# Performance work log

Measured on AMD Instinct MI355X. Metric: run time of the kernel, lower is better.

The kernel has to match this reference:

```python
import jax, jax.numpy as jnp
import numpy as np

B=2048; MA=6; S=11; SP=10; D=256; H=4; DH=64; L=12; G=2
NREL=500; NTYPE=1000; NODE=100000; VOC=NODE-NTYPE; NEDGE=100; E=50000; NCLS=NREL+NTYPE
BIG=1e6

def _ln(x, g, b, eps):
    m = jnp.mean(x, -1, keepdims=True)
    v = jnp.var(x, -1, keepdims=True)
    return (x - m) / jnp.sqrt(v + eps) * g + b

def _gat(h, bias, pos, Ws, a_src, a_dst):
    # h: [N,T,D]; bias: [N,T,T] additive mask; pos: [N,T,1] presence mask
    for i in range(Ws.shape[0]):
        hW = h @ Ws[i]                                   # [N,T,D]
        s = hW @ a_src[i]                                # [N,T]
        t = hW @ a_dst[i]                                # [N,T]
        e = jax.nn.leaky_relu(s[:, :, None] + t[:, None, :], 0.2) + bias
        attn = jax.nn.softmax(e, -1)
        h = jax.nn.elu(attn @ hW)
    denom = jnp.clip(jnp.sum(pos, 1), 1.0, None)         # [N,1]
    return jnp.sum(h * pos, 1) / denom                   # masked mean pool -> [N,D]

def _forward(input_ids, input_mask, edge_labels, mask_pos, mask_type, ent_types, groud_truth, l2m,
             node_emb, ln1_g, ln1_b, ln2_g, ln2_b, fc2_bias, fc3_bias, edge_k_emb, edge_v_emb,
             gat1_W, gat1_a_src, gat1_a_dst, gat2_W, gat2_a_src, gat2_a_dst,
             enc_wqkv, enc_wo, enc_ln1g, enc_ln1b, enc_w1, enc_b1, enc_w2, enc_b2, enc_ln2g, enc_ln2b):
    emb_out = _ln(node_emb[input_ids], ln1_g, ln1_b, 1e-12)   # dropout = identity (eval)
    # --- level-1 type hypergraph attention ---
    special = jnp.stack([jnp.full((SP,), 0), jnp.full((SP,), 1), jnp.full((SP,), 2)]).astype(ent_types.dtype)
    type_matrix = jnp.concatenate([special, ent_types[:, 1:]], 0)
    input_type_ids = input_ids[:, 0::2] - NREL                # [B,MA]
    itt = type_matrix[input_type_ids.reshape(-1)]             # [B*MA,SP]
    sgn = jnp.sign(itt).astype(jnp.float32)
    pos = sgn[:, :, None]
    bias = BIG * (pos @ jnp.swapaxes(pos, 1, 2) - 1.0)        # [N,SP,SP]
    input_type = node_emb[itt]                                # [N,SP,D]
    g1 = _gat(input_type, bias, pos, gat1_W, gat1_a_src, gat1_a_dst).reshape(B, MA, D)
    gathered = g1[:, l2m, :].reshape(B * MA, MA - 1, D)       # cross-arity gather
    tmp = jnp.abs(jnp.sum(gathered, 2))                       # [N,MA-1]
    h2 = jnp.concatenate([input_type, gathered], 1)           # [N,SP+MA-1,D]
    sgn2 = jnp.concatenate([sgn, jnp.sign(tmp)], 1)
    pos2 = sgn2[:, :, None]
    bias2 = BIG * (pos2 @ jnp.swapaxes(pos2, 1, 2) - 1.0)
    g2 = _gat(h2, bias2, pos2, gat2_W, gat2_a_src, gat2_a_dst).reshape(B, MA, D)
    emb_out = emb_out.at[:, 0::2, :].set(g2)                  # scatter types into entity slots
    mask_matrix = jnp.where(mask_type == 1, 2, 1)
    emb_out = emb_out.at[jnp.arange(B), mask_pos, :].set(node_emb[mask_matrix])
    # --- edge-aware transformer encoder (GRAN-style) ---
    em = jnp.sign(edge_labels).astype(jnp.float32)[..., None]
    ek = edge_k_emb[edge_labels] * em                          # [B,S,S,DH]
    ev = edge_v_emb[edge_labels] * em
    im = input_mask[:, :, None]
    am = (BIG * (im @ jnp.swapaxes(im, 1, 2) - 1.0))[:, None, :, :]  # [B,1,S,S]
    scale = 1.0 / np.sqrt(DH).astype(np.float32)
    def layer(x, p):
        wqkv, wo, l1g, l1b, w1, b1, w2, b2, l2g, l2b = p
        q, k, v = jnp.split(x @ wqkv, 3, -1)
        rs = lambda t: jnp.swapaxes(t.reshape(B, S, H, DH), 1, 2)
        q, k, v = rs(q), rs(k), rs(v)
        sc = (jnp.einsum('bhid,bhjd->bhij', q, k) + jnp.einsum('bhid,bijd->bhij', q, ek)) * scale + am
        at = jax.nn.softmax(sc, -1)
        ctx = jnp.einsum('bhij,bhjd->bhid', at, v) + jnp.einsum('bhij,bijd->bhid', at, ev)
        ctx = jnp.swapaxes(ctx, 1, 2).reshape(B, S, D) @ wo
        x = _ln(x + ctx, l1g, l1b, 1e-12)
        hf = jax.nn.gelu(x @ w1 + b1, approximate=False) @ w2 + b2
        x = _ln(x + hf, l2g, l2b, 1e-12)
        return x, None
    enc_out, _ = jax.lax.scan(layer, emb_out, (enc_wqkv, enc_wo, enc_ln1g, enc_ln1b, enc_w1, enc_b1, enc_w2, enc_b2, enc_ln2g, enc_ln2b))
    hm = enc_out[jnp.arange(B), mask_pos]                      # [B,D]
    hm = _ln(jax.nn.gelu(hm, approximate=False), ln2_g, ln2_b, 1e-7)
    fc1 = hm @ node_emb[VOC:NODE].T + fc3_bias                 # [B,NTYPE]
    fc2 = hm @ node_emb[3:3 + NREL].T + fc2_bias               # [B,NREL]
    fc_out = jnp.concatenate([fc2, fc1], 1)
    ind = jnp.concatenate([-jnp.ones((B, NREL)), jnp.ones((B, NTYPE))], 1) * mask_type[:, None].astype(jnp.float32)
    fc_out = fc_out + BIG * (jax.nn.relu(ind) - 1.0)
    rm = (mask_type == -1).astype(jnp.float32)
    tm = (mask_type == 1).astype(jnp.float32)
    rlab = groud_truth[:, :NREL]; rlab = rlab / jnp.sum(rlab, 1, keepdims=True)
    tlab = groud_truth[:, NREL:]; tlab = tlab / jnp.sum(tlab, 1, keepdims=True)
    ce_r = -jnp.sum(rlab * jax.nn.log_softmax(fc2, -1), 1)
    ce_t = -jnp.sum(tlab * jax.nn.log_softmax(fc1, -1), 1)
    loss = jnp.sum(rm * ce_r) / jnp.maximum(jnp.sum(rm), 1.0) + jnp.sum(tm * ce_t) / jnp.maximum(jnp.sum(tm), 1.0)
    return loss, fc_out

def setup_inputs():
    key = jax.random.key(0)
    ks = jax.random.split(key, 24)
    f = lambda k, shape: jax.random.normal(k, shape, jnp.float32) * 0.02
    inp = {}
    inp['input_ids'] = jax.random.randint(ks[0], (B, S), NREL, NREL + 3 + E)
    inp['input_mask'] = jnp.ones((B, S), jnp.float32)
    inp['edge_labels'] = jax.random.randint(ks[1], (B, S, S), 0, NEDGE)
    inp['mask_pos'] = jax.random.randint(ks[2], (B,), 0, S)
    inp['mask_label'] = jax.random.randint(ks[3], (B,), 0, NCLS)
    mt = jax.random.randint(ks[4], (B,), 0, 2) * 2 - 1
    inp['mask_type'] = mt.at[0].set(-1).at[1].set(1)
    inp['ent_types'] = jax.random.randint(ks[5], (E, SP + 1), VOC, NODE)
    gt = (jax.random.uniform(ks[6], (B, NCLS)) < 0.02).astype(jnp.float32)
    inp['groud_truth'] = gt.at[:, 0].set(1.0).at[:, NREL].set(1.0)
    inp['type_attn_l2_matrix'] = jnp.asarray(np.stack([[j for j in range(MA) if j != i] for i in range(MA)]))
    inp['node_emb'] = f(ks[7], (NODE, D))
    inp['ln1_g'] = jnp.ones((D,)); inp['ln1_b'] = jnp.zeros((D,))
    inp['ln2_g'] = jnp.ones((D,)); inp['ln2_b'] = jnp.zeros((D,))
    inp['fc2_bias'] = jnp.zeros((NREL,)); inp['fc3_bias'] = jnp.zeros((NTYPE,))
    inp['edge_k_emb'] = f(ks[8], (NEDGE, DH)); inp['edge_v_emb'] = f(ks[9], (NEDGE, DH))
    inp['gat1_W'] = f(ks[10], (G, D, D)); inp['gat1_a_src'] = f(ks[11], (G, D)); inp['gat1_a_dst'] = f(ks[12], (G, D))
    inp['gat2_W'] = f(ks[13], (G, D, D)); inp['gat2_a_src'] = f(ks[14], (G, D)); inp['gat2_a_dst'] = f(ks[15], (G, D))
    inp['enc_wqkv'] = f(ks[16], (L, D, 3 * D)); inp['enc_wo'] = f(ks[17], (L, D, D))
    inp['enc_ln1g'] = jnp.ones((L, D)); inp['enc_ln1b'] = jnp.zeros((L, D))
    inp['enc_w1'] = f(ks[18], (L, D, 512)); inp['enc_b1'] = jnp.zeros((L, 512))
    inp['enc_w2'] = f(ks[19], (L, 512, D)); inp['enc_b2'] = jnp.zeros((L, D))
    inp['enc_ln2g'] = jnp.ones((L, D)); inp['enc_ln2b'] = jnp.zeros((L, D))
    return inp

def reference(input_ids, input_mask, edge_labels, mask_pos, mask_label, mask_type, ent_types, groud_truth, type_attn_l2_matrix,
              node_emb, ln1_g, ln1_b, ln2_g, ln2_b, fc2_bias, fc3_bias, edge_k_emb, edge_v_emb,
              gat1_W, gat1_a_src, gat1_a_dst, gat2_W, gat2_a_src, gat2_a_dst,
              enc_wqkv, enc_wo, enc_ln1g, enc_ln1b, enc_w1, enc_b1, enc_w2, enc_b2, enc_ln2g, enc_ln2b):
    return _forward(input_ids, input_mask, edge_labels, mask_pos, mask_type, ent_types, groud_truth, type_attn_l2_matrix,
                    node_emb, ln1_g, ln1_b, ln2_g, ln2_b, fc2_bias, fc3_bias, edge_k_emb, edge_v_emb,
                    gat1_W, gat1_a_src, gat1_a_dst, gat2_W, gat2_a_src, gat2_a_dst,
                    enc_wqkv, enc_wo, enc_ln1g, enc_ln1b, enc_w1, enc_b1, enc_w2, enc_b2, enc_ln2g, enc_ln2b)
```

## Files before the change

### kernel.cpp

```cpp
#include <hip/hip_runtime.h>
#include <math.h>

constexpr int CB=2048, CMA=6, CS=11, CSP=10, CD=256, CH=4, CDH=64, CL=12;
constexpr int CNREL=500, CNTYPE=1000, CNODE=100000, CVOC=99000, CNCLS=1500;
constexpr int NN  = CB*CMA;
constexpr int NSR = CB*CS;
constexpr int NTAB= 3+CNTYPE;
constexpr int GCH = 2048;
constexpr float BIGF = 1000000.0f;

typedef __attribute__((ext_vector_type(8))) short short8v;
typedef __attribute__((ext_vector_type(4))) float f32x4;
typedef unsigned short ushort;

__device__ __forceinline__ float lreluf(float x){ return x>=0.f ? x : 0.2f*x; }
__device__ __forceinline__ float eluf1(float x){ return x>0.f ? x : expm1f(x); }
__device__ __forceinline__ float geluf(float x){ return 0.5f*x*(1.f+erff(x*0.70710678118654752f)); }

__device__ __forceinline__ ushort f2bf(float v){
  unsigned u = __float_as_uint(v);
  unsigned r = (u + 0x7FFFu + ((u>>16)&1u)) >> 16;
  return (ushort)r;
}
__device__ __forceinline__ float bf2f(ushort s){ return __uint_as_float(((unsigned)s)<<16); }
// ... 20 lines not shown

__global__ __launch_bounds__(256)
void k_wsplit(const float* __restrict__ src0, ushort* __restrict__ dst0, int K, int N)
{
  __shared__ float t[32][33];
  const int z = blockIdx.z;
  const float* src = src0 + (size_t)z*K*N;
  ushort* hi = dst0 + (size_t)z*2*K*N;
  ushort* lo = hi + (size_t)K*N;
  const int nb = blockIdx.x*32, kb = blockIdx.y*32;
  const int r = threadIdx.x>>5, c = threadIdx.x&31;
#pragma unroll
  for (int i=0;i<4;i++)
    t[r+8*i][c] = src[(size_t)(kb + r + 8*i)*N + nb + c];
  __syncthreads();
#pragma unroll
  for (int i=0;i<4;i++){
    int lin = threadIdx.x + 256*i;
    int n = lin>>5, k = lin&31;
    float v = t[k][n];
    ushort h, l; split2(v, h, l);
    hi[(size_t)(nb+n)*K + kb + k] = h;
    lo[(size_t)(nb+n)*K + kb + k] = l;
  }
}

template<int EPI, bool BIAS>
__global__ __launch_bounds__(256,2)
void k_mgemm(const ushort* __restrict__ Ahi, const ushort* __restrict__ Alo,
             const ushort* __restrict__ Bhi, const ushort* __restrict__ Blo,
             const float* __restrict__ bias, const float* __restrict__ res,
             const float* __restrict__ lng, const float* __restrict__ lnb,
             float* __restrict__ C, ushort* __restrict__ Chi, ushort* __restrict__ Clo,
             int M, int N, int K)
{
  constexpr int LDK = 40;
  __shared__ alignas(16) ushort Ash[2][64*LDK];
  __shared__ alignas(16) ushort Bsh[2][256*LDK];
  const int tid = threadIdx.x;
  const int wv = tid>>6, ln = tid&63;
  const int fr = ln&15, fq = ln>>4;
  const int bm = blockIdx.y*64, bn = blockIdx.x*256;
  f32x4 acc[4][4];
#pragma unroll
  for (int m=0;m<4;m++)
#pragma unroll
    for (int n=0;n<4;n++) acc[m][n] = (f32x4){0.f,0.f,0.f,0.f};

  for (int k0=0;k0<K;k0+=32){
    __syncthreads();
#pragma unroll
    for (int s=0;s<10;s++){
      int u = tid + s*256;
      const ushort* gp; ushort* lp;
      if (u < 512){
        int hl = u>>8, r = (u>>2)&63, ko = (u&3)*8;
        gp = (hl ? Alo : Ahi) + (size_t)(bm+r)*K + k0 + ko;
        lp = &Ash[hl][r*LDK + ko];
      } else {
        int u2 = u - 512;
        int hl = u2>>10, r = (u2>>2)&255, ko = (u2&3)*8;
        gp = (hl ? Blo : Bhi) + (size_t)(bn+r)*K + k0 + ko;
        lp = &Bsh[hl][r*LDK + ko];
      }
      *(short8v*)lp = *(const short8v*)gp;
    }
// ... 76 lines not shown
    float* redS = (float*)&Ash[0][0];
    if (fr==0){
#pragma unroll
      for (int m=0;m<4;m++)
#pragma unroll
        for (int j=0;j<4;j++){
          int r = m*16 + fq*4 + j;
          redS[wv*64 + r] = sum_[m][j];
          redS[256 + wv*64 + r] = sq_[m][j];
        }
    }
    __syncthreads();
#pragma unroll
    for (int m=0;m<4;m++)
#pragma unroll
      for (int j=0;j<4;j++){
        int r = m*16 + fq*4 + j;
        float S = redS[r] + redS[64+r] + redS[128+r] + redS[192+r];
        float Q = redS[256+r] + redS[320+r] + redS[384+r] + redS[448+r];
        float mean = S*(1.f/256.f);
        float var  = Q*(1.f/256.f) - mean*mean;
        float rstd = 1.f/sqrtf(var + 1e-12f);
        size_t ro = (size_t)(bm + r)*256;
#pragma unroll
        for (int n=0;n<4;n++){
          int col = wv*64 + n*16 + fr;
          float o = (acc[m][n][j] - mean)*rstd*gcol[n] + bbcol[n];
          C[ro + col] = o;
          ushort hh,ll; split2(o,hh,ll);
          Chi[ro+col]=hh; Clo[ro+col]=ll;
        }
      }
  }
}

__global__ __launch_bounds__(256)
void k_typeprep(const int* __restrict__ input_ids, const int* __restrict__ ent_types,
                int* __restrict__ itt)
{
  int idx = blockIdx.x*256 + threadIdx.x;
  if (idx >= NN*CSP) return;
  int n = idx / CSP, sp = idx % CSP;
  int b = n / CMA, ma = n % CMA;
  int id = input_ids[b*CS + 2*ma] - CNREL;
  itt[idx] = (id < 3) ? id : ent_types[(size_t)(id-3)*(CSP+1) + sp + 1];
}

__global__ __launch_bounds__(256)
void k_tables(const float* __restrict__ emb, const float* __restrict__ W,
              const float* __restrict__ asrc, const float* __restrict__ adst,
              float* __restrict__ TW, float* __restrict__ Ts, float* __restrict__ Tt)
{
  __shared__ float row[CD];
  __shared__ float red[8];
  const int r = blockIdx.x, d = threadIdx.x;
  const int nrow = (r<3) ? r : (CVOC + (r-3));
  row[d] = emb[(size_t)nrow*CD + d];
  __syncthreads();
  float acc = 0.f;
  for (int k=0;k<CD;k+=4){
    const float4 hv = *reinterpret_cast<const float4*>(&row[k]);
    acc = fmaf(hv.x, W[(size_t)(k+0)*CD+d],
          fmaf(hv.y, W[(size_t)(k+1)*CD+d],
          fmaf(hv.z, W[(size_t)(k+2)*CD+d],
          fmaf(hv.w, W[(size_t)(k+3)*CD+d], acc))));
  }
  TW[(size_t)r*CD+d] = acc;
  float s = blk_sum(acc*asrc[d], red);
  float t = blk_sum(acc*adst[d], red);
  if (d==0){ Ts[r]=s; Tt[r]=t; }
}

template<int ACT, bool BIAS>
__global__ __launch_bounds__(256)
void k_gemm128(const float* __restrict__ A, const float* __restrict__ Bm,
               const float* __restrict__ bias, float* __restrict__ C,
               int M, int N, int K)
{
  __shared__ alignas(16) float As[16][132];
  __shared__ alignas(16) float Bs[16][132];
  const int tid = threadIdx.x;
  const int bn = blockIdx.x*128, bm = blockIdx.y*128;
  const int tx = tid & 15, ty = tid >> 4;
  const int ar = tid >> 1, ak = (tid & 1)*8;
  const int bk = tid >> 4, bnl = (tid & 15)*8;
  const float* Ap = A + (size_t)(bm + ar)*K + ak;
  const float* Bp = Bm + (size_t)bk*N + bn + bnl;
  float acc[8][8] = {};
  for (int k0=0; k0<K; k0+=16){
    float4 av0 = *reinterpret_cast<const float4*>(Ap + k0);
    float4 av1 = *reinterpret_cast<const float4*>(Ap + k0 + 4);
    float4 bv0 = *reinterpret_cast<const float4*>(Bp + (size_t)k0*N);
    float4 bv1 = *reinterpret_cast<const float4*>(Bp + (size_t)k0*N + 4);
    __syncthreads();
    As[ak+0][ar]=av0.x; As[ak+1][ar]=av0.y; As[ak+2][ar]=av0.z; As[ak+3][ar]=av0.w;
    As[ak+4][ar]=av1.x; As[ak+5][ar]=av1.y; As[ak+6][ar]=av1.z; As[ak+7][ar]=av1.w;
    *reinterpret_cast<float4*>(&Bs[bk][bnl])   = bv0;
    *reinterpret_cast<float4*>(&Bs[bk][bnl+4]) = bv1;
    __syncthreads();
#pragma unroll
    for (int kk=0; kk<16; kk++){
      float a_[8], b_[8];
      *reinterpret_cast<float4*>(&a_[0]) = *reinterpret_cast<const float4*>(&As[kk][ty*8]);
      *reinterpret_cast<float4*>(&a_[4]) = *reinterpret_cast<const float4*>(&As[kk][ty*8+4]);
      *reinterpret_cast<float4*>(&b_[0]) = *reinterpret_cast<const float4*>(&Bs[kk][tx*8]);
      *reinterpret_cast<float4*>(&b_[4]) = *reinterpret_cast<const float4*>(&Bs[kk][tx*8+4]);
#pragma unroll
      for (int i=0;i<8;i++)
#pragma unroll
        for (int j=0;j<8;j++) acc[i][j] = fmaf(a_[i], b_[j], acc[i][j]);
    }
  }
#pragma unroll
  for (int i=0;i<8;i++){
    const int row = bm + ty*8 + i;
    float outv[8];
#pragma unroll
    for (int j=0;j<8;j++){
      float v = acc[i][j];
      if (BIAS) v += bias[bn + tx*8 + j];
      if (ACT==1) v = geluf(v);
      outv[j] = v;
    }
    *reinterpret_cast<float4*>(C + (size_t)row*N + bn + tx*8)     = *reinterpret_cast<float4*>(&outv[0]);
    *reinterpret_cast<float4*>(C + (size_t)row*N + bn + tx*8 + 4) = *reinterpret_cast<float4*>(&outv[4]);
  }
}

__global__ __launch_bounds__(256)
void k_g1red(const float* __restrict__ g1, const float* __restrict__ GW,
             const float* __restrict__ asrc, const float* __restrict__ adst,
             float* __restrict__ Gs, float* __restrict__ Gt, float* __restrict__ Grs)
{
  __shared__ float red[8];
  const int n = blockIdx.x, d = threadIdx.x;
  float w = GW[(size_t)n*CD + d];
  float v = g1[(size_t)n*CD + d];
  float s  = blk_sum(w*asrc[d], red);
  float t  = blk_sum(w*adst[d], red);
  float rs = blk_sum(v, red);
  if (d==0){ Gs[n]=s; Gt[n]=t; Grs[n]=rs; }
}

template<int P>
__device__ __forceinline__ void gat_softmax(float (*att)[P+1], const float* sA,
                                            const float* tA, const int* sg)
{
  const int i = threadIdx.x;
  if (i < P){
    if (sg[i]){
      float si = sA[i];
      float e[P];
      float m = -3.0e38f;
#pragma unroll
      for (int j=0;j<P;j++){
        e[j] = 0.f;
        if (sg[j]){ e[j] = lreluf(si + tA[j]); m = fmaxf(m, e[j]); }
      }
      float s = 0.f;
#pragma unroll
      for (int j=0;j<P;j++){
        float w = sg[j] ? expf(e[j]-m) : 0.f;
        att[i][j] = w; s += w;
      }
      float inv = 1.f/s;
#pragma unroll
      for (int j=0;j<P;j++) att[i][j] *= inv;
    } else {
#pragma unroll
      for (int j=0;j<P;j++) att[i][j] = 0.f;
    }
  }
}

template<int P>
__global__ __launch_bounds__(256)
void k_gatl1(int nbase, const int* __restrict__ itt,
             const float* __restrict__ TW, const float* __restrict__ Ts, const float* __restrict__ Tt,
             const float* __restrict__ GW, const float* __restrict__ Gs, const float* __restrict__ Gt,
             const float* __restrict__ Grs, const int* __restrict__ l2m,
             ushort* __restrict__ H1hi, ushort* __restrict__ H1lo)
{
  __shared__ float hW[P][CD];
  __shared__ float att[P][P+1];
  __shared__ float sA[P], tA[P];
  __shared__ int sg[P], ridx[P];
  const int n = nbase + blockIdx.x;
  const int d = threadIdx.x;
  if (d < P){
    if (d < CSP){
      int it = itt[n*CSP + d];
      int r = (it < 3) ? it : (it - (CVOC - 3));
      ridx[d]=r; sg[d]=(it>0); sA[d]=Ts[r]; tA[d]=Tt[r];
    } else {
      int ma = n % CMA;
      int m = l2m[ma*(CMA-1) + (d - CSP)];
      int nb = (n / CMA)*CMA + m;
      ridx[d]=nb; sg[d]=(Grs[nb]!=0.f); sA[d]=Gs[nb]; tA[d]=Gt[nb];
    }
  }
  __syncthreads();
#pragma unroll
  for (int i=0;i<P;i++){
    const float* src = (i<CSP) ? TW : GW;
    hW[i][d] = src[(size_t)ridx[i]*CD + d];
  }
  __syncthreads();
  gat_softmax<P>(att, sA, tA, sg);
  __syncthreads();
  float h[P];
#pragma unroll
  for (int i=0;i<P;i++) h[i]=0.f;
#pragma unroll
  for (int j=0;j<P;j++){
    float w = hW[j][d];
#pragma unroll
    for (int i=0;i<P;i++) h[i] = fmaf(att[i][j], w, h[i]);
  }
  size_t rb = ((size_t)blockIdx.x*P)*CD + d;
#pragma unroll
  for (int i=0;i<P;i++){
    float e = eluf1(h[i]);
    ushort hh,ll; split2(e,hh,ll);
    H1hi[rb + (size_t)i*CD] = hh;
    H1lo[rb + (size_t)i*CD] = ll;
  }
}

template<int P>
__global__ __launch_bounds__(256)
void k_gatl2(int nbase, const int* __restrict__ itt, const float* __restrict__ Grs,
             const int* __restrict__ l2m, const float* __restrict__ Z,
             const float* __restrict__ as2, const float* __restrict__ ad2,
             float* __restrict__ gout)
{
  __shared__ float zb[P][CD];
  __shared__ float att[P][P+1];
  __shared__ float sA[P], tA[P];
  __shared__ int sg[P];
  const int n = nbase + blockIdx.x;
  const int d = threadIdx.x;
  size_t zrow = (size_t)blockIdx.x*P*CD;
#pragma unroll
  for (int i=0;i<P;i++) zb[i][d] = Z[zrow + (size_t)i*CD + d];
  if (d < P){
    if (d < CSP) sg[d] = (itt[n*CSP + d] > 0);
    else {
      int ma = n % CMA;
      int m = l2m[ma*(CMA-1) + (d - CSP)];
      int nb = (n / CMA)*CMA + m;
      sg[d] = (Grs[nb] != 0.f);
    }
  }
  __syncthreads();
  {
    int i = d>>4, l = d&15;
    if (i < P){
      float ps=0.f, pt=0.f;
      for (int dd=l; dd<CD; dd+=16){
        float w = zb[i][dd];
        ps = fmaf(w, as2[dd], ps);
        pt = fmaf(w, ad2[dd], pt);
      }
#pragma unroll
      for (int o=8;o;o>>=1){ ps += __shfl_down(ps,o,16); pt += __shfl_down(pt,o,16); }
      if (l==0){ sA[i]=ps; tA[i]=pt; }
    }
  }
  __syncthreads();
  gat_softmax<P>(att, sA, tA, sg);
  __syncthreads();
  float x[P];
#pragma unroll
  for (int i=0;i<P;i++) x[i]=0.f;
#pragma unroll
  for (int j=0;j<P;j++){
    float w = zb[j][d];
#pragma unroll
    for (int i=0;i<P;i++) x[i] = fmaf(att[i][j], w, x[i]);
  }
  float den=0.f;
#pragma unroll
  for (int i=0;i<P;i++) den += (float)sg[i];
  den = fmaxf(den,1.f);
  float o=0.f;
#pragma unroll
  for (int i=0;i<P;i++) if (sg[i]) o += eluf1(x[i]);
  gout[(size_t)n*CD + d] = o/den;
}

__global__ __launch_bounds__(256)
void k_x0(const int* __restrict__ input_ids, const int* __restrict__ mask_pos,
          const int* __restrict__ mask_type, const float* __restrict__ emb,
          const float* __restrict__ g2, const float* __restrict__ g,
          const float* __restrict__ bta, float* __restrict__ x,
          ushort* __restrict__ xhi, ushort* __restrict__ xlo)
{
  __shared__ float red[8];
  const int row = blockIdx.x;
  const int b = row / CS, s = row % CS;
  const int d = threadIdx.x;
  float val;
  if (s == mask_pos[b]){
    int mm = (mask_type[b]==1) ? 2 : 1;
    val = emb[(size_t)mm*CD + d];
  } else if ((s & 1) == 0){
    val = g2[(size_t)(b*CMA + (s>>1))*CD + d];
  } else {
    float v = emb[(size_t)input_ids[row]*CD + d];
    float m = blk_sum(v, red)*(1.f/CD);
    float dv = v - m;
    float var = blk_sum(dv*dv, red)*(1.f/CD);
    val = dv/sqrtf(var+1e-12f)*g[d] + bta[d];
  }
  size_t o = (size_t)row*CD + d;
  x[o] = val;
  ushort hh,ll; split2(val,hh,ll);
  xhi[o]=hh; xlo[o]=ll;
}

__global__ __launch_bounds__(128)
// ... 37 lines not shown
    at[i][j] = (accq + em*acce)*0.125f + amv;
  }
  __syncthreads();
  if (tid < CS){
    float m = -3.0e38f;
#pragma unroll
    for (int j=0;j<CS;j++) m = fmaxf(m, at[tid][j]);
    float e[CS]; float s = 0.f;
#pragma unroll
    for (int j=0;j<CS;j++){ e[j] = expf(at[tid][j]-m); s += e[j]; }
    float inv = 1.f/s;
#pragma unroll
    for (int j=0;j<CS;j++) at[tid][j] = e[j]*inv;
  }
  __syncthreads();
  for (int idx=tid; idx<CS*16; idx+=128){
    int i = idx>>4, d4 = idx&15;
    float4 a = {0.f,0.f,0.f,0.f};
#pragma unroll
    for (int j=0;j<CS;j++){
      float w = at[i][j];
      int l = lab[i*CS+j];
      float4 v4 = *reinterpret_cast<const float4*>(&vs[j][d4*4]);
      float4 e4 = *reinterpret_cast<const float4*>(evtab + (size_t)l*CDH + d4*4);
      float em = (l>0) ? 1.f : 0.f;
      a.x = fmaf(w, fmaf(em,e4.x,v4.x), a.x);
      a.y = fmaf(w, fmaf(em,e4.y,v4.y), a.y);
      a.z = fmaf(w, fmaf(em,e4.z,v4.z), a.z);
      a.w = fmaf(w, fmaf(em,e4.w,v4.w), a.w);
    }
    size_t o = ((size_t)b*CS + i)*CD + h*CDH + d4*4;
    ushort hh0,ll0,hh1,ll1,hh2,ll2,hh3,ll3;
    split2(a.x,hh0,ll0); split2(a.y,hh1,ll1); split2(a.z,hh2,ll2); split2(a.w,hh3,ll3);
    unsigned hi01 = (unsigned)hh0 | ((unsigned)hh1<<16);
    unsigned hi23 = (unsigned)hh2 | ((unsigned)hh3<<16);
    unsigned lo01 = (unsigned)ll0 | ((unsigned)ll1<<16);
    unsigned lo23 = (unsigned)ll2 | ((unsigned)ll3<<16);
    *reinterpret_cast<uint2*>(ctxhi + o) = make_uint2(hi01, hi23);
    *reinterpret_cast<uint2*>(ctxlo + o) = make_uint2(lo01, lo23);
  }
}

__global__ __launch_bounds__(256)
void k_head(const float* __restrict__ x, const int* __restrict__ mask_pos,
            const float* __restrict__ g, const float* __restrict__ bta,
            float* __restrict__ hm)
{
  __shared__ float red[8];
  const int b = blockIdx.x, d = threadIdx.x;
  float v = geluf(x[((size_t)b*CS + mask_pos[b])*CD + d]);
  float m = blk_sum(v, red)*(1.f/CD);
  float dv = v - m;
  float var = blk_sum(dv*dv, red)*(1.f/CD);
  hm[(size_t)b*CD + d] = dv/sqrtf(var+1e-7f)*g[d] + bta[d];
}

__global__ __launch_bounds__(256)
void k_fc(const float* __restrict__ hm, const float* __restrict__ emb,
          const float* __restrict__ fc2b, const float* __restrict__ fc3b,
          float* __restrict__ out)
{
  __shared__ alignas(16) float As[32][36];
  __shared__ alignas(16) float Bs[32][68];
  const int bn = blockIdx.x*64, bm = blockIdx.y*32;
  const int tid = threadIdx.x;
  const int tx = tid & 15, ty = tid >> 4;
  const int ar = tid >> 3, ak = (tid & 7)*4;
  const int bnl = tid >> 2, bk8 = (tid & 3)*8;
  const int c = bn + bnl;
  const float* brow = nullptr;
  if (c < CNCLS){
    int rr = (c < CNREL) ? (3 + c) : (CVOC + (c - CNREL));
// ... 97 lines not shown
  const int*   l2m        = (const int*)  d_in[8];
  const float* emb        = (const float*)d_in[9];
  const float* ln1g=(const float*)d_in[10], *ln1b=(const float*)d_in[11];
  const float* ln2g=(const float*)d_in[12], *ln2b=(const float*)d_in[13];
  const float* fc2b=(const float*)d_in[14], *fc3b=(const float*)d_in[15];
  const float* ektab=(const float*)d_in[16], *evtab=(const float*)d_in[17];
  const float* g1W=(const float*)d_in[18], *g1as=(const float*)d_in[19], *g1ad=(const float*)d_in[20];
  const float* g2W=(const float*)d_in[21], *g2as=(const float*)d_in[22], *g2ad=(const float*)d_in[23];
  const float* wqkv=(const float*)d_in[24], *wo=(const float*)d_in[25];
  const float* el1g=(const float*)d_in[26], *el1b=(const float*)d_in[27];
  const float* w1=(const float*)d_in[28], *b1=(const float*)d_in[29];
  const float* w2=(const float*)d_in[30], *b2=(const float*)d_in[31];
  const float* el2g=(const float*)d_in[32], *el2b=(const float*)d_in[33];

  char* wsb = (char*)d_ws;
  size_t off = 0;
  auto alloc = [&](size_t bytes)->char*{
    char* p = wsb + off;
    off += (bytes + 255) & ~(size_t)255;
    return p;
  };
  int*   itt  = (int*)  alloc((size_t)NN*CSP*4);
  float* TW1  = (float*)alloc((size_t)NTAB*CD*4);
  float* Ts1  = (float*)alloc(NTAB*4);
  float* Tt1  = (float*)alloc(NTAB*4);
  float* TW2  = (float*)alloc((size_t)NTAB*CD*4);
  float* Ts2  = (float*)alloc(NTAB*4);
  float* Tt2  = (float*)alloc(NTAB*4);
  float* g1o  = (float*)alloc((size_t)NN*CD*4);
  float* G1W  = (float*)alloc((size_t)NN*CD*4);
  float* G1s  = (float*)alloc(NN*4);
  float* G1t  = (float*)alloc(NN*4);
  float* G1rs = (float*)alloc(NN*4);
  float* xb   = (float*)alloc((size_t)NSR*CD*4);
  ushort* xhi = (ushort*)alloc((size_t)NSR*CD*2);
  ushort* xlo = (ushort*)alloc((size_t)NSR*CD*2);
  ushort* ctxhi = (ushort*)alloc((size_t)NSR*CD*2);
  ushort* ctxlo = (ushort*)alloc((size_t)NSR*CD*2);
  char*  qkvR = alloc((size_t)NSR*768*4);
  ushort* wbuf = (ushort*)alloc((size_t)12845056*2);
  float* hm   = (float*)alloc((size_t)CB*CD*4);
  float* cer  = (float*)alloc(CB*4);
  float* cet  = (float*)alloc(CB*4);

  float* qkvb = (float*)qkvR;
  ushort* H1hi = (ushort*)qkvR;
  ushort* H1lo = (ushort*)(qkvR + (size_t)16*1024*1024);
  float*  Zbuf = (float*)(qkvR + (size_t)32*1024*1024);
  ushort* ffhi = (ushort*)qkvR;
  ushort* fflo = (ushort*)(qkvR + (size_t)24*1024*1024);
  float* g2o = g1o;

  ushort* wqkvT = wbuf;
  ushort* woT   = wqkvT + (size_t)12*2*768*256;
  ushort* w1T   = woT   + (size_t)12*2*256*256;
  ushort* w2T   = w1T   + (size_t)12*2*512*256;
  ushort* g1wT  = w2T   + (size_t)12*2*256*512;
  ushort* g2wT  = g1wT  + (size_t)2*256*256;

  float* dout = (float*)d_out;
  float* fcp  = dout + 1;

  k_wsplit<<<dim3(24,8,12),dim3(256),0,stream>>>(wqkv, wqkvT, 256, 768);
  k_wsplit<<<dim3(8,8,12),dim3(256),0,stream>>>(wo, woT, 256, 256);
  k_wsplit<<<dim3(16,8,12),dim3(256),0,stream>>>(w1, w1T, 256, 512);
  k_wsplit<<<dim3(8,16,12),dim3(256),0,stream>>>(w2, w2T, 512, 256);
  k_wsplit<<<dim3(8,8,1),dim3(256),0,stream>>>(g1W + CD*CD, g1wT, 256, 256);
  k_wsplit<<<dim3(8,8,1),dim3(256),0,stream>>>(g2W + CD*CD, g2wT, 256, 256);

  k_typeprep<<<dim3((NN*CSP+255)/256),dim3(256),0,stream>>>(input_ids, ent_types, itt);
  k_tables<<<dim3(NTAB),dim3(256),0,stream>>>(emb, g1W, g1as, g1ad, TW1, Ts1, Tt1);
  k_tables<<<dim3(NTAB),dim3(256),0,stream>>>(emb, g2W, g2as, g2ad, TW2, Ts2, Tt2);
  for (int c=0;c<NN/GCH;c++){
    int nb0 = c*GCH;
    k_gatl1<10><<<dim3(GCH),dim3(256),0,stream>>>(nb0, itt, TW1, Ts1, Tt1,
        nullptr,nullptr,nullptr,nullptr,nullptr, H1hi, H1lo);
    k_mgemm<0,false><<<dim3(1,GCH*10/64),dim3(256),0,stream>>>(H1hi, H1lo, g1wT, g1wT+65536,
        nullptr,nullptr,nullptr,nullptr, Zbuf, nullptr,nullptr, GCH*10, 256, 256);
    k_gatl2<10><<<dim3(GCH),dim3(256),0,stream>>>(nb0, itt, nullptr, nullptr, Zbuf,
        g1as + CD, g1ad + CD, g1o);
  }
  k_gemm128<0,false><<<dim3(2,NN/128),dim3(256),0,stream>>>(g1o, g2W, nullptr, G1W, NN, 256, 256);
  k_g1red<<<dim3(NN),dim3(256),0,stream>>>(g1o, G1W, g2as, g2ad, G1s, G1t, G1rs);
  for (int c=0;c<NN/GCH;c++){
    int nb0 = c*GCH;
    k_gatl1<15><<<dim3(GCH),dim3(256),0,stream>>>(nb0, itt, TW2, Ts2, Tt2,
        G1W, G1s, G1t, G1rs, l2m, H1hi, H1lo);
    k_mgemm<0,false><<<dim3(1,GCH*15/64),dim3(256),0,stream>>>(H1hi, H1lo, g2wT, g2wT+65536,
        nullptr,nullptr,nullptr,nullptr, Zbuf, nullptr,nullptr, GCH*15, 256, 256);
    k_gatl2<15><<<dim3(GCH),dim3(256),0,stream>>>(nb0, itt, G1rs, l2m, Zbuf,
        g2as + CD, g2ad + CD, g2o);
  }
  k_x0<<<dim3(NSR),dim3(256),0,stream>>>(input_ids, mask_pos, mask_type, emb, g2o,
      ln1g, ln1b, xb, xhi, xlo);

  for (int l=0;l<CL;l++){
    const ushort* qh = wqkvT + (size_t)l*2*768*256; const ushort* ql = qh + 768*256;
    const ushort* oh = woT   + (size_t)l*2*256*256; const ushort* ol = oh + 256*256;
    const ushort* ah = w1T   + (size_t)l*2*512*256; const ushort* a2 = ah + 512*256;
    const ushort* bh = w2T   + (size_t)l*2*256*512; const ushort* b2l= bh + 256*512;
    k_mgemm<0,false><<<dim3(3,NSR/64),dim3(256),0,stream>>>(xhi, xlo, qh, ql,
        nullptr,nullptr,nullptr,nullptr, qkvb, nullptr,nullptr, NSR, 768, 256);
    k_attn<<<dim3(CB*CH),dim3(128),0,stream>>>(qkvb, edge_labels, ektab, evtab, input_mask,
        ctxhi, ctxlo);
    k_mgemm<2,false><<<dim3(1,NSR/64),dim3(256),0,stream>>>(ctxhi, ctxlo, oh, ol,
        nullptr, xb, el1g + (size_t)l*CD, el1b + (size_t)l*CD, xb, xhi, xlo, NSR, 256, 256);
    k_mgemm<1,true><<<dim3(2,NSR/64),dim3(256),0,stream>>>(xhi, xlo, ah, a2,
        b1 + (size_t)l*512, nullptr,nullptr,nullptr, nullptr, ffhi, fflo, NSR, 512, 256);
    k_mgemm<2,true><<<dim3(1,NSR/64),dim3(256),0,stream>>>(ffhi, fflo, bh, b2l,
        b2 + (size_t)l*CD, xb, el2g + (size_t)l*CD, el2b + (size_t)l*CD, xb, xhi, xlo, NSR, 256, 512);
  }

  k_head<<<dim3(CB),dim3(256),0,stream>>>(xb, mask_pos, ln2g, ln2b, hm);
  k_fc<<<dim3((CNCLS+63)/64, CB/32),dim3(256),0,stream>>>(hm, emb, fc2b, fc3b, fcp);
  k_ce<<<dim3(CB),dim3(256),0,stream>>>(fcp, gtruth, mask_type, cer, cet);
  k_loss<<<dim3(1),dim3(256),0,stream>>>(cer, cet, mask_type, dout);
}
```

Baseline: 3.664 ms.

## Fuse GAT attention-score dots into MFMA GEMM epilogue and warp-level GAT kernels

```diff
diff --git a/kernel.cpp b/kernel.cpp
--- a/kernel.cpp
+++ b/kernel.cpp
@@ -76,6 +76,7 @@
              const float* __restrict__ bias, const float* __restrict__ res,
              const float* __restrict__ lng, const float* __restrict__ lnb,
              float* __restrict__ C, ushort* __restrict__ Chi, ushort* __restrict__ Clo,
+             float* __restrict__ st_s, float* __restrict__ st_t,
              int M, int N, int K)
 {
   constexpr int LDK = 40;
@@ -218,6 +219,54 @@
         }
       }
   }
+  if constexpr (EPI == 3){
+    float ucol[4], vcol[4];
+#pragma unroll
+    for (int n=0;n<4;n++){
+      int col = wv*64 + n*16 + fr;
+      ucol[n] = lng[col]; vcol[n] = lnb[col];
+    }
+    float su[4][4], sv[4][4];
+#pragma unroll
+    for (int m=0;m<4;m++)
+#pragma unroll
+      for (int j=0;j<4;j++){
+        size_t ro = (size_t)(bm + m*16 + fq*4 + j)*256;
+        float s=0.f, q=0.f;
+#pragma unroll
+        for (int n=0;n<4;n++){
+          float f = acc[m][n][j];
+          C[ro + wv*64 + n*16 + fr] = f;
+          s = fmaf(f, ucol[n], s); q = fmaf(f, vcol[n], q);
+        }
+#pragma unroll
+        for (int o=1;o<16;o<<=1){ s += __shfl_xor(s,o,64); q += __shfl_xor(q,o,64); }
+        su[m][j]=s; sv[m][j]=q;
+      }
+    __syncthreads();
+    float* redS = (float*)&Ash[0][0];
+    if (fr==0){
+#pragma unroll
+      for (int m=0;m<4;m++)
+#pragma unroll
+        for (int j=0;j<4;j++){
+          int r = m*16 + fq*4 + j;
+          redS[wv*64 + r] = su[m][j];
+          redS[256 + wv*64 + r] = sv[m][j];
+        }
+    }
+    __syncthreads();
+    if (wv==0 && fr==0){
+#pragma unroll
+      for (int m=0;m<4;m++)
+#pragma unroll
+        for (int j=0;j<4;j++){
+          int r = m*16 + fq*4 + j;
+          st_s[bm+r] = redS[r] + redS[64+r] + redS[128+r] + redS[192+r];
+          st_t[bm+r] = redS[256+r] + redS[320+r] + redS[384+r] + redS[448+r];
+        }
+    }
+  }
 }
 
 __global__ __launch_bounds__(256)
@@ -257,222 +306,156 @@
   if (d==0){ Ts[r]=s; Tt[r]=t; }
 }
 
-template<int ACT, bool BIAS>
-__global__ __launch_bounds__(256)
-void k_gemm128(const float* __restrict__ A, const float* __restrict__ Bm,
-               const float* __restrict__ bias, float* __restrict__ C,
-               int M, int N, int K)
-{
-  __shared__ alignas(16) float As[16][132];
-  __shared__ alignas(16) float Bs[16][132];
-  const int tid = threadIdx.x;
-  const int bn = blockIdx.x*128, bm = blockIdx.y*128;
-  const int tx = tid & 15, ty = tid >> 4;
-  const int ar = tid >> 1, ak = (tid & 1)*8;
-  const int bk = tid >> 4, bnl = (tid & 15)*8;
-  const float* Ap = A + (size_t)(bm + ar)*K + ak;
-  const float* Bp = Bm + (size_t)bk*N + bn + bnl;
-  float acc[8][8] = {};
-  for (int k0=0; k0<K; k0+=16){
-    float4 av0 = *reinterpret_cast<const float4*>(Ap + k0);
-    float4 av1 = *reinterpret_cast<const float4*>(Ap + k0 + 4);
-    float4 bv0 = *reinterpret_cast<const float4*>(Bp + (size_t)k0*N);
-    float4 bv1 = *reinterpret_cast<const float4*>(Bp + (size_t)k0*N + 4);
-    __syncthreads();
-    As[ak+0][ar]=av0.x; As[ak+1][ar]=av0.y; As[ak+2][ar]=av0.z; As[ak+3][ar]=av0.w;
-    As[ak+4][ar]=av1.x; As[ak+5][ar]=av1.y; As[ak+6][ar]=av1.z; As[ak+7][ar]=av1.w;
-    *reinterpret_cast<float4*>(&Bs[bk][bnl])   = bv0;
-    *reinterpret_cast<float4*>(&Bs[bk][bnl+4]) = bv1;
-    __syncthreads();
-#pragma unroll
-    for (int kk=0; kk<16; kk++){
-      float a_[8], b_[8];
-      *reinterpret_cast<float4*>(&a_[0]) = *reinterpret_cast<const float4*>(&As[kk][ty*8]);
-      *reinterpret_cast<float4*>(&a_[4]) = *reinterpret_cast<const float4*>(&As[kk][ty*8+4]);
-      *reinterpret_cast<float4*>(&b_[0]) = *reinterpret_cast<const float4*>(&Bs[kk][tx*8]);
-      *reinterpret_cast<float4*>(&b_[4]) = *reinterpret_cast<const float4*>(&Bs[kk][tx*8+4]);
-#pragma unroll
-      for (int i=0;i<8;i++)
-#pragma unroll
-        for (int j=0;j<8;j++) acc[i][j] = fmaf(a_[i], b_[j], acc[i][j]);
-    }
-  }
-#pragma unroll
-  for (int i=0;i<8;i++){
-    const int row = bm + ty*8 + i;
-    float outv[8];
-#pragma unroll
-    for (int j=0;j<8;j++){
-      float v = acc[i][j];
-      if (BIAS) v += bias[bn + tx*8 + j];
-      if (ACT==1) v = geluf(v);
-      outv[j] = v;
-    }
-    *reinterpret_cast<float4*>(C + (size_t)row*N + bn + tx*8)     = *reinterpret_cast<float4*>(&outv[0]);
-    *reinterpret_cast<float4*>(C + (size_t)row*N + bn + tx*8 + 4) = *reinterpret_cast<float4*>(&outv[4]);
-  }
-}
-
-__global__ __launch_bounds__(256)
-void k_g1red(const float* __restrict__ g1, const float* __restrict__ GW,
-             const float* __restrict__ asrc, const float* __restrict__ adst,
-             float* __restrict__ Gs, float* __restrict__ Gt, float* __restrict__ Grs)
-{
-  __shared__ float red[8];
-  const int n = blockIdx.x, d = threadIdx.x;
-  float w = GW[(size_t)n*CD + d];
-  float v = g1[(size_t)n*CD + d];
-  float s  = blk_sum(w*asrc[d], red);
-  float t  = blk_sum(w*adst[d], red);
-  float rs = blk_sum(v, red);
-  if (d==0){ Gs[n]=s; Gt[n]=t; Grs[n]=rs; }
-}
-
 template<int P>
-__device__ __forceinline__ void gat_softmax(float (*att)[P+1], const float* sA,
-                                            const float* tA, const int* sg)
-{
-  const int i = threadIdx.x;
-  if (i < P){
-    if (sg[i]){
-      float si = sA[i];
-      float e[P];
-      float m = -3.0e38f;
-#pragma unroll
-      for (int j=0;j<P;j++){
-        e[j] = 0.f;
-        if (sg[j]){ e[j] = lreluf(si + tA[j]); m = fmaxf(m, e[j]); }
-      }
-      float s = 0.f;
-#pragma unroll
-      for (int j=0;j<P;j++){
-        float w = sg[j] ? expf(e[j]-m) : 0.f;
-        att[i][j] = w; s += w;
-      }
-      float inv = 1.f/s;
-#pragma unroll
-      for (int j=0;j<P;j++) att[i][j] *= inv;
-    } else {
-#pragma unroll
-      for (int j=0;j<P;j++) att[i][j] = 0.f;
-    }
-  }
-}
-
-template<int P>
-__global__ __launch_bounds__(256)
-void k_gatl1(int nbase, const int* __restrict__ itt,
+__global__ __launch_bounds__(256,4)
+void k_gatw1(int nbase, const int* __restrict__ itt,
              const float* __restrict__ TW, const float* __restrict__ Ts, const float* __restrict__ Tt,
              const float* __restrict__ GW, const float* __restrict__ Gs, const float* __restrict__ Gt,
              const float* __restrict__ Grs, const int* __restrict__ l2m,
              ushort* __restrict__ H1hi, ushort* __restrict__ H1lo)
 {
-  __shared__ float hW[P][CD];
-  __shared__ float att[P][P+1];
-  __shared__ float sA[P], tA[P];
-  __shared__ int sg[P], ridx[P];
-  const int n = nbase + blockIdx.x;
-  const int d = threadIdx.x;
-  if (d < P){
-    if (d < CSP){
-      int it = itt[n*CSP + d];
-      int r = (it < 3) ? it : (it - (CVOC - 3));
-      ridx[d]=r; sg[d]=(it>0); sA[d]=Ts[r]; tA[d]=Tt[r];
+  const int wv = threadIdx.x>>6, l = threadIdx.x&63;
+  const int nrel = blockIdx.x*4 + wv;
+  const int n = nbase + nrel;
+  const int j = l & 15;
+  int ridx=0, sg=0; float sv=0.f, tv=0.f;
+  if (j < P){
+    if (j < CSP){
+      int it = itt[n*CSP + j];
+      int r = (it<3) ? it : (it-(CVOC-3));
+      ridx=r; sg=(it>0); sv=Ts[r]; tv=Tt[r];
     } else {
       int ma = n % CMA;
-      int m = l2m[ma*(CMA-1) + (d - CSP)];
-      int nb = (n / CMA)*CMA + m;
-      ridx[d]=nb; sg[d]=(Grs[nb]!=0.f); sA[d]=Gs[nb]; tA[d]=Gt[nb];
-    }
-  }
-  __syncthreads();
+      int m = l2m[ma*(CMA-1) + (j-CSP)];
+      int nb = (n/CMA)*CMA + m;
+      ridx=nb; sg=(Grs[nb]!=0.f); sv=Gs[nb]; tv=Gt[nb];
+    }
+  }
+  float4 z[P];
 #pragma unroll
   for (int i=0;i<P;i++){
+    int ri = __shfl(ridx, i);
     const float* src = (i<CSP) ? TW : GW;
-    hW[i][d] = src[(size_t)ridx[i]*CD + d];
-  }
-  __syncthreads();
-  gat_softmax<P>(att, sA, tA, sg);
-  __syncthreads();
-  float h[P];
-#pragma unroll
-  for (int i=0;i<P;i++) h[i]=0.f;
-#pragma unroll
-  for (int j=0;j<P;j++){
-    float w = hW[j][d];
-#pragma unroll
-    for (int i=0;i<P;i++) h[i] = fmaf(att[i][j], w, h[i]);
-  }
-  size_t rb = ((size_t)blockIdx.x*P)*CD + d;
+    z[i] = *reinterpret_cast<const float4*>(src + (size_t)ri*CD + 4*l);
+  }
+  float att[P];
 #pragma unroll
   for (int i=0;i<P;i++){
-    float e = eluf1(h[i]);
-    ushort hh,ll; split2(e,hh,ll);
-    H1hi[rb + (size_t)i*CD] = hh;
-    H1lo[rb + (size_t)i*CD] = ll;
-  }
-}
-
-template<int P>
-__global__ __launch_bounds__(256)
-void k_gatl2(int nbase, const int* __restrict__ itt, const float* __restrict__ Grs,
+    float si = __shfl(sv, i);
+    int  sgi = __shfl(sg, i);
+    int act = sgi && sg && (j<P);
+    float e = act ? lreluf(si+tv) : -3.0e38f;
+    float m = e;
+#pragma unroll
+    for (int o=1;o<16;o<<=1) m = fmaxf(m, __shfl_xor(m,o,16));
+    float w = act ? expf(e-m) : 0.f;
+    float s = w;
+#pragma unroll
+    for (int o=1;o<16;o<<=1) s += __shfl_xor(s,o,16);
+    att[i] = sgi ? w*(1.f/s) : 0.f;
+  }
+  size_t rb = ((size_t)nrel*P)*CD + 4*l;
+#pragma unroll
+  for (int i=0;i<P;i++){
+    float4 x = {0.f,0.f,0.f,0.f};
+#pragma unroll
+    for (int jj=0;jj<P;jj++){
+      float a = __shfl(att[i], jj);
+      x.x = fmaf(a, z[jj].x, x.x);
+      x.y = fmaf(a, z[jj].y, x.y);
+      x.z = fmaf(a, z[jj].z, x.z);
+      x.w = fmaf(a, z[jj].w, x.w);
+    }
+    float e0=eluf1(x.x), e1=eluf1(x.y), e2=eluf1(x.z), e3=eluf1(x.w);
+    ushort h0,l0,h1,l1,h2,l2,h3,l3;
+    split2(e0,h0,l0); split2(e1,h1,l1); split2(e2,h2,l2); split2(e3,h3,l3);
+    size_t o = rb + (size_t)i*CD;
+    *reinterpret_cast<uint2*>(H1hi + o) = make_uint2((unsigned)h0|((unsigned)h1<<16), (unsigned)h2|((unsigned)h3<<16));
+    *reinterpret_cast<uint2*>(H1lo + o) = make_uint2((unsigned)l0|((unsigned)l1<<16), (unsigned)l2|((unsigned)l3<<16));
+  }
+}
+
+template<int P, bool SPLIT, bool WRS>
+__global__ __launch_bounds__(256,4)
+void k_gatw2(int nbase, const int* __restrict__ itt, const float* __restrict__ Grs_in,
              const int* __restrict__ l2m, const float* __restrict__ Z,
-             const float* __restrict__ as2, const float* __restrict__ ad2,
-             float* __restrict__ gout)
-{
-  __shared__ float zb[P][CD];
-  __shared__ float att[P][P+1];
-  __shared__ float sA[P], tA[P];
-  __shared__ int sg[P];
-  const int n = nbase + blockIdx.x;
-  const int d = threadIdx.x;
-  size_t zrow = (size_t)blockIdx.x*P*CD;
-#pragma unroll
-  for (int i=0;i<P;i++) zb[i][d] = Z[zrow + (size_t)i*CD + d];
-  if (d < P){
-    if (d < CSP) sg[d] = (itt[n*CSP + d] > 0);
+             const float* __restrict__ Zs, const float* __restrict__ Zt,
+             float* __restrict__ gout, ushort* __restrict__ ghi, ushort* __restrict__ glo,
+             float* __restrict__ Grs_out)
+{
+  const int wv = threadIdx.x>>6, l = threadIdx.x&63;
+  const int nrel = blockIdx.x*4 + wv;
+  const int n = nbase + nrel;
+  const int j = l & 15;
+  int sg=0; float sv=0.f, tv=0.f;
+  if (j < P){
+    if (j < CSP) sg = (itt[n*CSP + j] > 0);
     else {
       int ma = n % CMA;
-      int m = l2m[ma*(CMA-1) + (d - CSP)];
-      int nb = (n / CMA)*CMA + m;
-      sg[d] = (Grs[nb] != 0.f);
-    }
-  }
-  __syncthreads();
-  {
-    int i = d>>4, l = d&15;
-    if (i < P){
-      float ps=0.f, pt=0.f;
-      for (int dd=l; dd<CD; dd+=16){
-        float w = zb[i][dd];
-        ps = fmaf(w, as2[dd], ps);
-        pt = fmaf(w, ad2[dd], pt);
-      }
-#pragma unroll
-      for (int o=8;o;o>>=1){ ps += __shfl_down(ps,o,16); pt += __shfl_down(pt,o,16); }
-      if (l==0){ sA[i]=ps; tA[i]=pt; }
-    }
-  }
-  __syncthreads();
-  gat_softmax<P>(att, sA, tA, sg);
-  __syncthreads();
-  float x[P];
-#pragma unroll
-  for (int i=0;i<P;i++) x[i]=0.f;
-#pragma unroll
-  for (int j=0;j<P;j++){
-    float w = zb[j][d];
-#pragma unroll
-    for (int i=0;i<P;i++) x[i] = fmaf(att[i][j], w, x[i]);
-  }
-  float den=0.f;
-#pragma unroll
-  for (int i=0;i<P;i++) den += (float)sg[i];
-  den = fmaxf(den,1.f);
-  float o=0.f;
-#pragma unroll
-  for (int i=0;i<P;i++) if (sg[i]) o += eluf1(x[i]);
-  gout[(size_t)n*CD + d] = o/den;
+      int m = l2m[ma*(CMA-1) + (j-CSP)];
+      int nb = (n/CMA)*CMA + m;
+      sg = (Grs_in[nb] != 0.f);
+    }
+    sv = Zs[nrel*P + j]; tv = Zt[nrel*P + j];
+  }
+  float4 z[P];
+#pragma unroll
+  for (int i=0;i<P;i++)
+    z[i] = *reinterpret_cast<const float4*>(Z + ((size_t)nrel*P + i)*CD + 4*l);
+  float att[P];
+#pragma unroll
+  for (int i=0;i<P;i++){
+    float si = __shfl(sv, i);
+    int  sgi = __shfl(sg, i);
+    int act = sgi && sg && (j<P);
+    float e = act ? lreluf(si+tv) : -3.0e38f;
+    float m = e;
+#pragma unroll
+    for (int o=1;o<16;o<<=1) m = fmaxf(m, __shfl_xor(m,o,16));
+    float w = act ? expf(e-m) : 0.f;
+    float s = w;
+#pragma unroll
+    for (int o=1;o<16;o<<=1) s += __shfl_xor(s,o,16);
+    att[i] = sgi ? w*(1.f/s) : 0.f;
+  }
+  float den = (j<P) ? (float)sg : 0.f;
+#pragma unroll
+  for (int o=1;o<16;o<<=1) den += __shfl_xor(den,o,16);
+  den = fmaxf(den, 1.f);
+  float4 acc = {0.f,0.f,0.f,0.f};
+#pragma unroll
+  for (int i=0;i<P;i++){
+    float4 x = {0.f,0.f,0.f,0.f};
+#pragma unroll
+    for (int jj=0;jj<P;jj++){
+      float a = __shfl(att[i], jj);
+      x.x = fmaf(a, z[jj].x, x.x);
+      x.y = fmaf(a, z[jj].y, x.y);
+      x.z = fmaf(a, z[jj].z, x.z);
+      x.w = fmaf(a, z[jj].w, x.w);
+    }
+    int sgi = __shfl(sg, i);
+    if (sgi){
+      acc.x += eluf1(x.x); acc.y += eluf1(x.y);
+      acc.z += eluf1(x.z); acc.w += eluf1(x.w);
+    }
+  }
+  float inv = 1.f/den;
+  acc.x *= inv; acc.y *= inv; acc.z *= inv; acc.w *= inv;
+  *reinterpret_cast<float4*>(gout + (size_t)n*CD + 4*l) = acc;
+  if constexpr (SPLIT){
+    ushort h0,l0,h1,l1,h2,l2,h3,l3;
+    split2(acc.x,h0,l0); split2(acc.y,h1,l1); split2(acc.z,h2,l2); split2(acc.w,h3,l3);
+    size_t o = (size_t)n*CD + 4*l;
+    *reinterpret_cast<uint2*>(ghi + o) = make_uint2((unsigned)h0|((unsigned)h1<<16), (unsigned)h2|((unsigned)h3<<16));
+    *reinterpret_cast<uint2*>(glo + o) = make_uint2((unsigned)l0|((unsigned)l1<<16), (unsigned)l2|((unsigned)l3<<16));
+  }
+  if constexpr (WRS){
+    float tot = acc.x + acc.y + acc.z + acc.w;
+#pragma unroll
+    for (int o=1;o<64;o<<=1) tot += __shfl_xor(tot,o,64);
+    if (l==0) Grs_out[n] = tot;
+  }
 }
 
 __global__ __launch_bounds__(256)
@@ -576,12 +559,8 @@
     size_t o = ((size_t)b*CS + i)*CD + h*CDH + d4*4;
     ushort hh0,ll0,hh1,ll1,hh2,ll2,hh3,ll3;
     split2(a.x,hh0,ll0); split2(a.y,hh1,ll1); split2(a.z,hh2,ll2); split2(a.w,hh3,ll3);
-    unsigned hi01 = (unsigned)hh0 | ((unsigned)hh1<<16);
-    unsigned hi23 = (unsigned)hh2 | ((unsigned)hh3<<16);
-    unsigned lo01 = (unsigned)ll0 | ((unsigned)ll1<<16);
-    unsigned lo23 = (unsigned)ll2 | ((unsigned)ll3<<16);
-    *reinterpret_cast<uint2*>(ctxhi + o) = make_uint2(hi01, hi23);
-    *reinterpret_cast<uint2*>(ctxlo + o) = make_uint2(lo01, lo23);
+    *reinterpret_cast<uint2*>(ctxhi + o) = make_uint2((unsigned)hh0|((unsigned)hh1<<16), (unsigned)hh2|((unsigned)hh3<<16));
+    *reinterpret_cast<uint2*>(ctxlo + o) = make_uint2((unsigned)ll0|((unsigned)ll1<<16), (unsigned)ll2|((unsigned)ll3<<16));
   }
 }
 
@@ -745,13 +724,17 @@
   float* G1s  = (float*)alloc(NN*4);
   float* G1t  = (float*)alloc(NN*4);
   float* G1rs = (float*)alloc(NN*4);
+  ushort* g1hi = (ushort*)alloc((size_t)NN*CD*2);
+  ushort* g1lo = (ushort*)alloc((size_t)NN*CD*2);
+  float* Zs   = (float*)alloc((size_t)GCH*15*4);
+  float* Zt   = (float*)alloc((size_t)GCH*15*4);
   float* xb   = (float*)alloc((size_t)NSR*CD*4);
   ushort* xhi = (ushort*)alloc((size_t)NSR*CD*2);
   ushort* xlo = (ushort*)alloc((size_t)NSR*CD*2);
   ushort* ctxhi = (ushort*)alloc((size_t)NSR*CD*2);
   ushort* ctxlo = (ushort*)alloc((size_t)NSR*CD*2);
   char*  qkvR = alloc((size_t)NSR*768*4);
-  ushort* wbuf = (ushort*)alloc((size_t)12845056*2);
+  ushort* wbuf = (ushort*)alloc((size_t)12976128*2);
   float* hm   = (float*)alloc((size_t)CB*CD*4);
   float* cer  = (float*)alloc(CB*4);
   float* cet  = (float*)alloc(CB*4);
@@ -770,6 +753,7 @@
   ushort* w2T   = w1T   + (size_t)12*2*512*256;
   ushort* g1wT  = w2T   + (size_t)12*2*256*512;
   ushort* g2wT  = g1wT  + (size_t)2*256*256;
+  ushort* g2w0T = g2wT  + (size_t)2*256*256;
 
   float* dout = (float*)d_out;
   float* fcp  = dout + 1;
@@ -780,29 +764,30 @@
   k_wsplit<<<dim3(8,16,12),dim3(256),0,stream>>>(w2, w2T, 512, 256);
   k_wsplit<<<dim3(8,8,1),dim3(256),0,stream>>>(g1W + CD*CD, g1wT, 256, 256);
   k_wsplit<<<dim3(8,8,1),dim3(256),0,stream>>>(g2W + CD*CD, g2wT, 256, 256);
+  k_wsplit<<<dim3(8,8,1),dim3(256),0,stream>>>(g2W, g2w0T, 256, 256);
 
   k_typeprep<<<dim3((NN*CSP+255)/256),dim3(256),0,stream>>>(input_ids, ent_types, itt);
   k_tables<<<dim3(NTAB),dim3(256),0,stream>>>(emb, g1W, g1as, g1ad, TW1, Ts1, Tt1);
   k_tables<<<dim3(NTAB),dim3(256),0,stream>>>(emb, g2W, g2as, g2ad, TW2, Ts2, Tt2);
   for (int c=0;c<NN/GCH;c++){
     int nb0 = c*GCH;
-    k_gatl1<10><<<dim3(GCH),dim3(256),0,stream>>>(nb0, itt, TW1, Ts1, Tt1,
+    k_gatw1<10><<<dim3(GCH/4),dim3(256),0,stream>>>(nb0, itt, TW1, Ts1, Tt1,
         nullptr,nullptr,nullptr,nullptr,nullptr, H1hi, H1lo);
-    k_mgemm<0,false><<<dim3(1,GCH*10/64),dim3(256),0,stream>>>(H1hi, H1lo, g1wT, g1wT+65536,
-        nullptr,nullptr,nullptr,nullptr, Zbuf, nullptr,nullptr, GCH*10, 256, 256);
-    k_gatl2<10><<<dim3(GCH),dim3(256),0,stream>>>(nb0, itt, nullptr, nullptr, Zbuf,
-        g1as + CD, g1ad + CD, g1o);
-  }
-  k_gemm128<0,false><<<dim3(2,NN/128),dim3(256),0,stream>>>(g1o, g2W, nullptr, G1W, NN, 256, 256);
-  k_g1red<<<dim3(NN),dim3(256),0,stream>>>(g1o, G1W, g2as, g2ad, G1s, G1t, G1rs);
+    k_mgemm<3,false><<<dim3(1,GCH*10/64),dim3(256),0,stream>>>(H1hi, H1lo, g1wT, g1wT+65536,
+        nullptr,nullptr, g1as + CD, g1ad + CD, Zbuf, nullptr,nullptr, Zs, Zt, GCH*10, 256, 256);
+    k_gatw2<10,true,true><<<dim3(GCH/4),dim3(256),0,stream>>>(nb0, itt, nullptr, nullptr,
+        Zbuf, Zs, Zt, g1o, g1hi, g1lo, G1rs);
+  }
+  k_mgemm<3,false><<<dim3(1,NN/64),dim3(256),0,stream>>>(g1hi, g1lo, g2w0T, g2w0T+65536,
+      nullptr,nullptr, g2as, g2ad, G1W, nullptr,nullptr, G1s, G1t, NN, 256, 256);
   for (int c=0;c<NN/GCH;c++){
     int nb0 = c*GCH;
-    k_gatl1<15><<<dim3(GCH),dim3(256),0,stream>>>(nb0, itt, TW2, Ts2, Tt2,
+    k_gatw1<15><<<dim3(GCH/4),dim3(256),0,stream>>>(nb0, itt, TW2, Ts2, Tt2,
         G1W, G1s, G1t, G1rs, l2m, H1hi, H1lo);
-    k_mgemm<0,false><<<dim3(1,GCH*15/64),dim3(256),0,stream>>>(H1hi, H1lo, g2wT, g2wT+65536,
-        nullptr,nullptr,nullptr,nullptr, Zbuf, nullptr,nullptr, GCH*15, 256, 256);
-    k_gatl2<15><<<dim3(GCH),dim3(256),0,stream>>>(nb0, itt, G1rs, l2m, Zbuf,
-        g2as + CD, g2ad + CD, g2o);
+    k_mgemm<3,false><<<dim3(1,GCH*15/64),dim3(256),0,stream>>>(H1hi, H1lo, g2wT, g2wT+65536,
+        nullptr,nullptr, g2as + CD, g2ad + CD, Zbuf, nullptr,nullptr, Zs, Zt, GCH*15, 256, 256);
+    k_gatw2<15,false,false><<<dim3(GCH/4),dim3(256),0,stream>>>(nb0, itt, G1rs, l2m,
+        Zbuf, Zs, Zt, g2o, nullptr, nullptr, nullptr);
   }
   k_x0<<<dim3(NSR),dim3(256),0,stream>>>(input_ids, mask_pos, mask_type, emb, g2o,
       ln1g, ln1b, xb, xhi, xlo);
@@ -813,15 +798,15 @@
     const ushort* ah = w1T   + (size_t)l*2*512*256; const ushort* a2 = ah + 512*256;
     const ushort* bh = w2T   + (size_t)l*2*256*512; const ushort* b2l= bh + 256*512;
     k_mgemm<0,false><<<dim3(3,NSR/64),dim3(256),0,stream>>>(xhi, xlo, qh, ql,
-        nullptr,nullptr,nullptr,nullptr, qkvb, nullptr,nullptr, NSR, 768, 256);
+        nullptr,nullptr,nullptr,nullptr, qkvb, nullptr,nullptr, nullptr,nullptr, NSR, 768, 256);
     k_attn<<<dim3(CB*CH),dim3(128),0,stream>>>(qkvb, edge_labels, ektab, evtab, input_mask,
         ctxhi, ctxlo);
     k_mgemm<2,false><<<dim3(1,NSR/64),dim3(256),0,stream>>>(ctxhi, ctxlo, oh, ol,
-        nullptr, xb, el1g + (size_t)l*CD, el1b + (size_t)l*CD, xb, xhi, xlo, NSR, 256, 256);
+        nullptr, xb, el1g + (size_t)l*CD, el1b + (size_t)l*CD, xb, xhi, xlo, nullptr,nullptr, NSR, 256, 256);
     k_mgemm<1,true><<<dim3(2,NSR/64),dim3(256),0,stream>>>(xhi, xlo, ah, a2,
-        b1 + (size_t)l*512, nullptr,nullptr,nullptr, nullptr, ffhi, fflo, NSR, 512, 256);
+        b1 + (size_t)l*512, nullptr,nullptr,nullptr, nullptr, ffhi, fflo, nullptr,nullptr, NSR, 512, 256);
     k_mgemm<2,true><<<dim3(1,NSR/64),dim3(256),0,stream>>>(ffhi, fflo, bh, b2l,
-        b2 + (size_t)l*CD, xb, el2g + (size_t)l*CD, el2b + (size_t)l*CD, xb, xhi, xlo, NSR, 256, 512);
+        b2 + (size_t)l*CD, xb, el2g + (size_t)l*CD, el2b + (size_t)l*CD, xb, xhi, xlo, nullptr,nullptr, NSR, 256, 512);
   }
 
   k_head<<<dim3(CB),dim3(256),0,stream>>>(xb, mask_pos, ln2g, ln2b, hm);
```

After: 3.334 ms. 9.0% less time.
